# Kernel optimization log

Hardware: AMD Instinct MI355X
Metric: run time of the kernel (lower is better)

The kernel has to match this reference:

```python
import jax, jax.numpy as jnp
import numpy as np

PAD = 8192          # padding index == bloom_filter_dim
H1, H2 = 512, 64
B, K, L = 32, 32, 128


def prelu(x, alpha):
    return jnp.where(x >= 0, x, alpha * x)


def embedding_bag_mean(w, idx):
    # EmbeddingBag(mode='mean', padding_idx=PAD): mean over non-padding entries
    emb = w[idx]                                   # [..., L, H1]
    m = (idx != PAD)[..., None].astype(w.dtype)    # [..., L, 1]
    s = (emb * m).sum(axis=-2)
    cnt = m.sum(axis=-2)
    return jnp.where(cnt > 0, s / jnp.maximum(cnt, 1.0), 0.0)


def hidden_layers(x, W1, b1, W2, b2, a0, a1, a2):
    # PReLU -> Linear -> PReLU -> Linear -> PReLU
    h = prelu(x, a0)
    h = prelu(h @ W1 + b1, a1)
    h = prelu(h @ W2 + b2, a2)
    return h


def setup_inputs() -> dict:
    key = jax.random.key(0)
    ks = jax.random.split(key, 16)
    f = lambda i, shape: jax.random.normal(ks[i], shape, dtype=jnp.float32) * 0.05
    s = lambda v: jnp.asarray(v, dtype=jnp.float32)
    return {
        'query_bloom_filter': jax.random.randint(ks[0], (B, L), 0, PAD),
        'poi_bloom_filter': jax.random.randint(ks[1], (B, K, L), 0, PAD),
        'query_loc': jax.random.normal(ks[2], (B, 2), dtype=jnp.float32),
        'poi_loc': jax.random.normal(ks[3], (B, K, 2), dtype=jnp.float32),
        'codebook_w': f(4, (PAD + 1, H1)),
        'q_W1': f(5, (H1, H2)), 'q_b1': f(6, (H2,)),
        'q_W2': f(7, (H2, H2)), 'q_b2': f(8, (H2,)),
        'p_W1': f(9, (H1, H2)), 'p_b1': f(10, (H2,)),
        'p_W2': f(11, (H2, H2)), 'p_b2': f(12, (H2,)),
        'q_eval_w': f(13, (PAD + 1, H2)),
        'p_eval_w': f(14, (PAD + 1, H2)),
        'q_a0': s(0.25), 'q_a1': s(0.25), 'q_a2': s(0.25),
        'p_a0': s(0.25), 'p_a1': s(0.25), 'p_a2': s(0.25),
        'ind_a': s(0.25),
        'a': s(1.0), 'b': s(0.0), 'c': s(1.0), 'd': s(0.0),
    }


def reference(query_bloom_filter, poi_bloom_filter, query_loc, poi_loc,
              codebook_w, q_W1, q_b1, q_W2, q_b2, p_W1, p_b1, p_W2, p_b2,
              q_eval_w, p_eval_w, q_a0, q_a1, q_a2, p_a0, p_a1, p_a2,
              ind_a, a, b, c, d):
    # --- dense towers ---
    query_embedding = embedding_bag_mean(codebook_w, query_bloom_filter)      # [B, H1]
    query_hidden = hidden_layers(query_embedding, q_W1, q_b1, q_W2, q_b2,
                                 q_a0, q_a1, q_a2)                            # [B, H2]
    poi_embedding = embedding_bag_mean(codebook_w, poi_bloom_filter)          # [B, K, H1]
    poi_hidden = hidden_layers(poi_embedding, p_W1, p_b1, p_W2, p_b2,
                               p_a0, p_a1, p_a2)                              # [B, K, H2]

    # --- bloom-filter intersection (isin_cuda): q element present in poi set ---
    q = query_bloom_filter[:, None, :]                                        # [B, 1, L]
    p = poi_bloom_filter                                                      # [B, K, L]
    match = (q[..., :, None] == p[..., None, :]) & (p[..., None, :] != PAD)   # [B, K, L, L]
    intersection_mask = match.any(axis=-1)                                    # [B, K, L]
    intersection = jnp.where(intersection_mask, q, PAD)                       # [B, K, L]

    # --- sparse term weights via evaluator gathers + mul-sum ---
    q_cols = q_eval_w[intersection]                                           # [B, K, L, H2]
    p_cols = p_eval_w[intersection]                                           # [B, K, L, H2]
    q_sw = prelu(jnp.einsum('bh,bklh->bkl', query_hidden, q_cols), ind_a) + 1.0
    p_sw = prelu(jnp.einsum('bkh,bklh->bkl', poi_hidden, p_cols), ind_a) + 1.0

    text_sim = jnp.where(intersection_mask, q_sw * p_sw, 0.0).sum(axis=-1)    # [B, K]

    # --- location similarity ---
    dist = jnp.sqrt(((query_loc[:, None, :] - poi_loc) ** 2).sum(axis=-1))    # [B, K]
    dist_sim = -jnp.log(dist + 1.0)

    # --- text-sim normalization + relevance ---
    max_sim = text_sim.max(axis=-1, keepdims=True)
    text_sim = (2.0 * text_sim - max_sim) / (max_sim + 1e-6)
    relevance_score = (c - jax.nn.sigmoid(a * text_sim + b)) * (dist_sim - d)
    return relevance_score
```

## Files before the change

### kernel.cpp

```cpp
#include <hip/hip_runtime.h>

#define PAD_V 8192
#define H1 512
#define H2 64
#define B_SZ 32
#define K_SZ 32
#define L_SZ 128
#define EMB_BLOCKS (B_SZ + B_SZ * K_SZ)
#define ISECT_BLOCKS ((B_SZ * K_SZ) / 4)

__global__ __launch_bounds__(512, 4) void front_kernel(
    const int* __restrict__ qbf, const int* __restrict__ pbf,
    const float* __restrict__ codebook,
    const float* __restrict__ qW1, const float* __restrict__ qb1,
    const float* __restrict__ qW2, const float* __restrict__ qb2,
    const float* __restrict__ pW1, const float* __restrict__ pb1,
    const float* __restrict__ pW2, const float* __restrict__ pb2,
    const float* __restrict__ qa0p, const float* __restrict__ qa1p, const float* __restrict__ qa2p,
    const float* __restrict__ pa0p, const float* __restrict__ pa1p, const float* __restrict__ pa2p,
    float* __restrict__ qh_out, float* __restrict__ ph_out,
    int* __restrict__ nh_ws, int* __restrict__ hits_ws)
{
    const int tid = threadIdx.x;

    if (blockIdx.x >= EMB_BLOCKS) {
        __shared__ unsigned int bm4[4][256];
        __shared__ int s_nh4[4];
        __shared__ int s_hit4[4][L_SZ];

        const int pair0 = (blockIdx.x - EMB_BLOCKS) * 4;
        const int sub = tid >> 7;
        const int t   = tid & 127;
        const int pair = pair0 + sub;
        const int b = pair >> 5;

        bm4[sub][t] = 0u; bm4[sub][t + 128] = 0u;
        if (t == 0) s_nh4[sub] = 0;
        __syncthreads();

        int pv = pbf[pair * L_SZ + t];
        if ((unsigned)pv < (unsigned)PAD_V)
            atomicOr(&bm4[sub][pv >> 5], 1u << (pv & 31));
        __syncthreads();

        int v = qbf[b * L_SZ + t];
        bool hit = ((unsigned)v < (unsigned)PAD_V) &&
                   ((bm4[sub][v >> 5] >> (v & 31)) & 1u);
        if (hit) {
            int pos = atomicAdd(&s_nh4[sub], 1);
            s_hit4[sub][pos] = v;
        }
        __syncthreads();

        if (t == 0) nh_ws[pair] = s_nh4[sub];
        if (t < s_nh4[sub]) hits_ws[pair * L_SZ + t] = s_hit4[sub][t];
        return;
    }

    const bool is_q = (blockIdx.x < B_SZ);
    const int* idx_base;
    int bag;
    const float *W1, *b1, *W2, *b2;
    float a0, a1, a2;
    float* out;
    if (is_q) {
        idx_base = qbf; bag = blockIdx.x;
        W1 = qW1; b1 = qb1; W2 = qW2; b2 = qb2;
        a0 = *qa0p; a1 = *qa1p; a2 = *qa2p;
        out = qh_out;
    } else {
        idx_base = pbf; bag = blockIdx.x - B_SZ;
        W1 = pW1; b1 = pb1; W2 = pW2; b2 = pb2;
        a0 = *pa0p; a1 = *pa1p; a2 = *pa2p;
        out = ph_out;
    }

    __shared__ int   s_idx[L_SZ];
    __shared__ int   s_cntp[2];
    __shared__ float s_red[3][L_SZ][4];
    __shared__ float s_x[H1];
    __shared__ float s_p1[32][H2];
    __shared__ float s_h1[H2];

    if (tid < L_SZ) s_idx[tid] = idx_base[bag * L_SZ + tid];
    __syncthreads();

    if (tid < L_SZ) {
        unsigned long long bal = __ballot(s_idx[tid] != PAD_V);
        if ((tid & 63) == 0) s_cntp[tid >> 6] = __popcll(bal);
    }

    const int g = tid & 127;
    const int q = tid >> 7;
    const float4* cb4 = (const float4*)codebook;
    float ax = 0.f, ay = 0.f, az = 0.f, aw = 0.f;
    {
        int   idx[8];
        float4 buf[8];
        #pragma unroll
        for (int batch = 0; batch < 4; batch++) {
            #pragma unroll
            for (int j = 0; j < 8; j++) idx[j] = s_idx[q * 32 + batch * 8 + j];
            #pragma unroll
            for (int j = 0; j < 8; j++) buf[j] = cb4[(size_t)idx[j] * 128 + g];
            #pragma unroll
            for (int j = 0; j < 8; j++) {
                float m = (idx[j] != PAD_V) ? 1.0f : 0.0f;
                ax = fmaf(m, buf[j].x, ax);
                ay = fmaf(m, buf[j].y, ay);
                az = fmaf(m, buf[j].z, az);
                aw = fmaf(m, buf[j].w, aw);
            }
        }
    }
    if (q != 0) {
        s_red[q - 1][g][0] = ax; s_red[q - 1][g][1] = ay;
        s_red[q - 1][g][2] = az; s_red[q - 1][g][3] = aw;
    }
    __syncthreads();
    if (q == 0) {
        int cnt = s_cntp[0] + s_cntp[1];
        float inv = (cnt > 0) ? 1.0f / (float)cnt : 0.0f;
        float e0 = (ax + s_red[0][g][0] + s_red[1][g][0] + s_red[2][g][0]) * inv;
        float e1 = (ay + s_red[0][g][1] + s_red[1][g][1] + s_red[2][g][1]) * inv;
        float e2 = (az + s_red[0][g][2] + s_red[1][g][2] + s_red[2][g][2]) * inv;
        float e3 = (aw + s_red[0][g][3] + s_red[1][g][3] + s_red[2][g][3]) * inv;
        s_x[4 * g + 0] = (e0 >= 0.f) ? e0 : a0 * e0;
        s_x[4 * g + 1] = (e1 >= 0.f) ? e1 : a0 * e1;
        s_x[4 * g + 2] = (e2 >= 0.f) ? e2 : a0 * e2;
        s_x[4 * g + 3] = (e3 >= 0.f) ? e3 : a0 * e3;
    }
    __syncthreads();

    const int j4 = tid & 15;
    const int ch = tid >> 4;
    const float4* W1v = (const float4*)W1;
    {
        const int i0 = ch * 16;
        float sx = 0.f, sy = 0.f, sz = 0.f, sw = 0.f;
        #pragma unroll
        for (int i = 0; i < 16; i++) {
            float x = s_x[i0 + i];
            float4 w = W1v[(size_t)(i0 + i) * 16 + j4];
            sx = fmaf(x, w.x, sx);
            sy = fmaf(x, w.y, sy);
            sz = fmaf(x, w.z, sz);
            sw = fmaf(x, w.w, sw);
        }
        s_p1[ch][4 * j4 + 0] = sx;
        s_p1[ch][4 * j4 + 1] = sy;
        s_p1[ch][4 * j4 + 2] = sz;
        s_p1[ch][4 * j4 + 3] = sw;
    }
    __syncthreads();
    if (tid < H2) {
        float s = b1[tid];
        #pragma unroll
        for (int r = 0; r < 32; r++) s += s_p1[r][tid];
        s_h1[tid] = (s >= 0.f) ? s : a1 * s;
    }
    __syncthreads();

    const float4* W2v = (const float4*)W2;
    {
        const int i0 = ch * 2;
        float sx = 0.f, sy = 0.f, sz = 0.f, sw = 0.f;
        #pragma unroll
        for (int i = 0; i < 2; i++) {
            float x = s_h1[i0 + i];
            float4 w = W2v[(size_t)(i0 + i) * 16 + j4];
            sx = fmaf(x, w.x, sx);
            sy = fmaf(x, w.y, sy);
            sz = fmaf(x, w.z, sz);
            sw = fmaf(x, w.w, sw);
        }
        s_p1[ch][4 * j4 + 0] = sx;
        s_p1[ch][4 * j4 + 1] = sy;
        s_p1[ch][4 * j4 + 2] = sz;
        s_p1[ch][4 * j4 + 3] = sw;
    }
    __syncthreads();
    if (tid < H2) {
        float s = b2[tid];
        #pragma unroll
        for (int r = 0; r < 32; r++) s += s_p1[r][tid];
        s = (s >= 0.f) ? s : a2 * s;
        out[bag * H2 + tid] = s;
    }
}

__global__ __launch_bounds__(64) void text_sim_kernel(
    const float* __restrict__ q_eval, const float* __restrict__ p_eval,
    const float* __restrict__ qh_ws, const float* __restrict__ ph_ws,
    const int* __restrict__ nh_ws, const int* __restrict__ hits_ws,
    const float* __restrict__ ind_ap,
    float* __restrict__ text_out)
{
    const int blk = blockIdx.x;
    const int b    = blk >> 5;
    const int lane = threadIdx.x;

    const float qh = qh_ws[b * H2 + lane];
    const float ph = ph_ws[blk * H2 + lane];
    const int   nh = nh_ws[blk];
    const float ind_a = *ind_ap;

    float local = 0.f;
    for (int hh = 0; hh < nh; hh++) {
        int v = hits_ws[blk * L_SZ + hh];
        float qd = qh * q_eval[(size_t)v * H2 + lane];
        float pd = ph * p_eval[(size_t)v * H2 + lane];
        #pragma unroll
        for (int m = 1; m < 64; m <<= 1) {
            qd += __shfl_xor(qd, m);
            pd += __shfl_xor(pd, m);
        }
        qd = (qd >= 0.f) ? qd : ind_a * qd;
        pd = (pd >= 0.f) ? pd : ind_a * pd;
        local += (qd + 1.f) * (pd + 1.f);
    }
    if (lane == 0) text_out[blk] = local;
}

__global__ __launch_bounds__(64) void epilogue_kernel(
    const float* __restrict__ text_ws,
    const float* __restrict__ qloc, const float* __restrict__ ploc,
    const float* __restrict__ ap, const float* __restrict__ bp,
    const float* __restrict__ cp, const float* __restrict__ dp,
    float* __restrict__ out)
{
    const int b = blockIdx.x;
    const int t = threadIdx.x;
    const int kk = t & 31;

    float ts_raw = text_ws[b * K_SZ + kk];
    float mx = ts_raw;
    #pragma unroll
    for (int m = 1; m < 32; m <<= 1) mx = fmaxf(mx, __shfl_xor(mx, m));

    float qx = qloc[b * 2], qy = qloc[b * 2 + 1];
    float px = ploc[(b * K_SZ + kk) * 2];
    float py = ploc[(b * K_SZ + kk) * 2 + 1];
    float dx = qx - px, dy = qy - py;
    float dist = sqrtf(dx * dx + dy * dy);
    float ds = -logf(dist + 1.0f);

    float ts = (2.0f * ts_raw - mx) / (mx + 1e-6f);
    float A = *ap, Bb = *bp, C = *cp, D = *dp;
    float sig = 1.0f / (1.0f + expf(-(A * ts + Bb)));
    if (t < 32) out[b * K_SZ + kk] = (C - sig) * (ds - D);
}

extern "C" void kernel_launch(void* const* d_in, const int* in_sizes, int n_in,
                              void* d_out, int out_size, void* d_ws, size_t ws_size,
                              hipStream_t stream) {
    const int*   qbf      = (const int*)d_in[0];
    const int*   pbf      = (const int*)d_in[1];
    const float* qloc     = (const float*)d_in[2];
    const float* ploc     = (const float*)d_in[3];
    const float* codebook = (const float*)d_in[4];
    const float* qW1      = (const float*)d_in[5];
    const float* qb1      = (const float*)d_in[6];
    const float* qW2      = (const float*)d_in[7];
    const float* qb2      = (const float*)d_in[8];
    const float* pW1      = (const float*)d_in[9];
    const float* pb1      = (const float*)d_in[10];
    const float* pW2      = (const float*)d_in[11];
    const float* pb2      = (const float*)d_in[12];
    const float* q_eval   = (const float*)d_in[13];
    const float* p_eval   = (const float*)d_in[14];
    const float* qa0      = (const float*)d_in[15];
    const float* qa1      = (const float*)d_in[16];
    const float* qa2      = (const float*)d_in[17];
    const float* pa0      = (const float*)d_in[18];
    const float* pa1      = (const float*)d_in[19];
    const float* pa2      = (const float*)d_in[20];
    const float* ind_a    = (const float*)d_in[21];
    const float* a        = (const float*)d_in[22];
    const float* bsc      = (const float*)d_in[23];
    const float* c        = (const float*)d_in[24];
    const float* d        = (const float*)d_in[25];

    float* qh   = (float*)d_ws;
    float* ph   = qh + B_SZ * H2;
    float* text = ph + B_SZ * K_SZ * H2;
    int*   nh   = (int*)(text + B_SZ * K_SZ);
    int*   hits = nh + B_SZ * K_SZ;

    front_kernel<<<EMB_BLOCKS + ISECT_BLOCKS, 512, 0, stream>>>(
        qbf, pbf, codebook,
        qW1, qb1, qW2, qb2, pW1, pb1, pW2, pb2,
        qa0, qa1, qa2, pa0, pa1, pa2,
        qh, ph, nh, hits);

    text_sim_kernel<<<B_SZ * K_SZ, 64, 0, stream>>>(
        q_eval, p_eval, qh, ph, nh, hits, ind_a, text);

    epilogue_kernel<<<B_SZ, 64, 0, stream>>>(
        text, qloc, ploc, a, bsc, c, d, (float*)d_out);
}
```

Before: 157.3 us.

## Split fused front kernel into sliced gather kernel and separate MLP kernel

Splits the embedding-bag gather from the MLP tower. The gather now runs as 8 column-slice blocks per bag with 256 threads each, which gives far more blocks and more memory-level parallelism across the codebook reads. The mean-pooled PReLU activations go to a workspace buffer, and a separate MLP kernel with 256 threads per block reads them back. The intersection blocks now handle 2 pairs each instead of 4. The cost is an extra kernel launch and a global round-trip for the 512-wide activations.

```diff
diff --git a/kernel.cpp b/kernel.cpp
--- a/kernel.cpp
+++ b/kernel.cpp
@@ -6,140 +6,164 @@
 #define B_SZ 32
 #define K_SZ 32
 #define L_SZ 128
-#define EMB_BLOCKS (B_SZ + B_SZ * K_SZ)
-#define ISECT_BLOCKS ((B_SZ * K_SZ) / 4)
-
-__global__ __launch_bounds__(512, 4) void front_kernel(
+#define NBAGS (B_SZ + B_SZ * K_SZ)
+#define NSLICE 8
+#define GATHER_BLOCKS (NBAGS * NSLICE)
+#define ISECT2_BLOCKS ((B_SZ * K_SZ) / 2)
+
+
+__global__ __launch_bounds__(256, 4) void gather_kernel(
     const int* __restrict__ qbf, const int* __restrict__ pbf,
     const float* __restrict__ codebook,
+    const float* __restrict__ qa0p, const float* __restrict__ pa0p,
+    float* __restrict__ x_ws,
+    int* __restrict__ nh_ws, int* __restrict__ hits_ws)
+{
+    const int tid = threadIdx.x;
+
+    if (blockIdx.x >= GATHER_BLOCKS) {
+        __shared__ unsigned int bm2[2][256];
+        __shared__ int s_nh2[2];
+        __shared__ int s_hit2[2][L_SZ];
+
+        const int pair0 = (blockIdx.x - GATHER_BLOCKS) * 2;
+        const int sub = tid >> 7;
+        const int t   = tid & 127;
+        const int pair = pair0 + sub;
+        const int b = pair >> 5;
+
+        bm2[sub][t] = 0u; bm2[sub][t + 128] = 0u;
+        if (t == 0) s_nh2[sub] = 0;
+        __syncthreads();
+
+        int pv = pbf[pair * L_SZ + t];
+        if ((unsigned)pv < (unsigned)PAD_V)
+            atomicOr(&bm2[sub][pv >> 5], 1u << (pv & 31));
+        __syncthreads();
+
+        int v = qbf[b * L_SZ + t];
+        bool hit = ((unsigned)v < (unsigned)PAD_V) &&
+                   ((bm2[sub][v >> 5] >> (v & 31)) & 1u);
+        if (hit) {
+            int pos = atomicAdd(&s_nh2[sub], 1);
+            s_hit2[sub][pos] = v;
+        }
+        __syncthreads();
+
+        if (t == 0) nh_ws[pair] = s_nh2[sub];
+        if (t < s_nh2[sub]) hits_ws[pair * L_SZ + t] = s_hit2[sub][t];
+        return;
+    }
+
+    const int slice = blockIdx.x & (NSLICE - 1);
+    const int bag   = blockIdx.x >> 3;
+    const bool is_q = (bag < B_SZ);
+    const int* idx_base = is_q ? qbf : pbf;
+    const int  bagl     = is_q ? bag : (bag - B_SZ);
+    const float a0      = is_q ? *qa0p : *pa0p;
+
+    __shared__ int   s_idx[L_SZ];
+    __shared__ int   s_cnt[2];
+    __shared__ float4 s_part[16][16];
+
+    if (tid < L_SZ) {
+        int v = idx_base[bagl * L_SZ + tid];
+        s_idx[tid] = v;
+        unsigned long long bal = __ballot(v != PAD_V);
+        if ((tid & 63) == 0) s_cnt[tid >> 6] = __popcll(bal);
+    }
+    __syncthreads();
+
+    const int c  = tid & 15;
+    const int r0 = tid >> 4;
+    const int gc = slice * 16 + c;
+    const float4* cb4 = (const float4*)codebook;
+
+    float ax = 0.f, ay = 0.f, az = 0.f, aw = 0.f;
+    {
+        int    idx[8];
+        float4 buf[8];
+        #pragma unroll
+        for (int j = 0; j < 8; j++) idx[j] = s_idx[r0 * 8 + j];
+        #pragma unroll
+        for (int j = 0; j < 8; j++) buf[j] = cb4[(size_t)idx[j] * 128 + gc];
+        #pragma unroll
+        for (int j = 0; j < 8; j++) {
+            float m = (idx[j] != PAD_V) ? 1.0f : 0.0f;
+            ax = fmaf(m, buf[j].x, ax);
+            ay = fmaf(m, buf[j].y, ay);
+            az = fmaf(m, buf[j].z, az);
+            aw = fmaf(m, buf[j].w, aw);
+        }
+    }
+    s_part[r0][c] = make_float4(ax, ay, az, aw);
+    __syncthreads();
+
+    if (tid < 16) {
+        int cnt = s_cnt[0] + s_cnt[1];
+        float inv = (cnt > 0) ? 1.0f / (float)cnt : 0.0f;
+        float e0 = 0.f, e1 = 0.f, e2 = 0.f, e3 = 0.f;
+        #pragma unroll
+        for (int r = 0; r < 16; r++) {
+            float4 p = s_part[r][tid];
+            e0 += p.x; e1 += p.y; e2 += p.z; e3 += p.w;
+        }
+        e0 *= inv; e1 *= inv; e2 *= inv; e3 *= inv;
+        float4 o;
+        o.x = (e0 >= 0.f) ? e0 : a0 * e0;
+        o.y = (e1 >= 0.f) ? e1 : a0 * e1;
+        o.z = (e2 >= 0.f) ? e2 : a0 * e2;
+        o.w = (e3 >= 0.f) ? e3 : a0 * e3;
+        ((float4*)x_ws)[(size_t)bag * 128 + slice * 16 + tid] = o;
+    }
+}
+
+__global__ __launch_bounds__(256, 8) void mlp_kernel(
+    const float* __restrict__ x_ws,
     const float* __restrict__ qW1, const float* __restrict__ qb1,
     const float* __restrict__ qW2, const float* __restrict__ qb2,
     const float* __restrict__ pW1, const float* __restrict__ pb1,
     const float* __restrict__ pW2, const float* __restrict__ pb2,
-    const float* __restrict__ qa0p, const float* __restrict__ qa1p, const float* __restrict__ qa2p,
-    const float* __restrict__ pa0p, const float* __restrict__ pa1p, const float* __restrict__ pa2p,
-    float* __restrict__ qh_out, float* __restrict__ ph_out,
-    int* __restrict__ nh_ws, int* __restrict__ hits_ws)
+    const float* __restrict__ qa1p, const float* __restrict__ qa2p,
+    const float* __restrict__ pa1p, const float* __restrict__ pa2p,
+    float* __restrict__ qh_out, float* __restrict__ ph_out)
 {
     const int tid = threadIdx.x;
-
-    if (blockIdx.x >= EMB_BLOCKS) {
-        __shared__ unsigned int bm4[4][256];
-        __shared__ int s_nh4[4];
-        __shared__ int s_hit4[4][L_SZ];
-
-        const int pair0 = (blockIdx.x - EMB_BLOCKS) * 4;
-        const int sub = tid >> 7;
-        const int t   = tid & 127;
-        const int pair = pair0 + sub;
-        const int b = pair >> 5;
-
-        bm4[sub][t] = 0u; bm4[sub][t + 128] = 0u;
-        if (t == 0) s_nh4[sub] = 0;
-        __syncthreads();
-
-        int pv = pbf[pair * L_SZ + t];
-        if ((unsigned)pv < (unsigned)PAD_V)
-            atomicOr(&bm4[sub][pv >> 5], 1u << (pv & 31));
-        __syncthreads();
-
-        int v = qbf[b * L_SZ + t];
-        bool hit = ((unsigned)v < (unsigned)PAD_V) &&
-                   ((bm4[sub][v >> 5] >> (v & 31)) & 1u);
-        if (hit) {
-            int pos = atomicAdd(&s_nh4[sub], 1);
-            s_hit4[sub][pos] = v;
-        }
-        __syncthreads();
-
-        if (t == 0) nh_ws[pair] = s_nh4[sub];
-        if (t < s_nh4[sub]) hits_ws[pair * L_SZ + t] = s_hit4[sub][t];
-        return;
-    }
-
-    const bool is_q = (blockIdx.x < B_SZ);
-    const int* idx_base;
-    int bag;
+    const int bag = blockIdx.x;
+    const bool is_q = (bag < B_SZ);
     const float *W1, *b1, *W2, *b2;
-    float a0, a1, a2;
+    float a1, a2;
     float* out;
+    int bagl;
     if (is_q) {
-        idx_base = qbf; bag = blockIdx.x;
+        bagl = bag;
         W1 = qW1; b1 = qb1; W2 = qW2; b2 = qb2;
-        a0 = *qa0p; a1 = *qa1p; a2 = *qa2p;
+        a1 = *qa1p; a2 = *qa2p;
         out = qh_out;
     } else {
-        idx_base = pbf; bag = blockIdx.x - B_SZ;
+        bagl = bag - B_SZ;
         W1 = pW1; b1 = pb1; W2 = pW2; b2 = pb2;
-        a0 = *pa0p; a1 = *pa1p; a2 = *pa2p;
+        a1 = *pa1p; a2 = *pa2p;
         out = ph_out;
     }
 
-    __shared__ int   s_idx[L_SZ];
-    __shared__ int   s_cntp[2];
-    __shared__ float s_red[3][L_SZ][4];
     __shared__ float s_x[H1];
-    __shared__ float s_p1[32][H2];
+    __shared__ float s_p1[16][H2];
     __shared__ float s_h1[H2];
 
-    if (tid < L_SZ) s_idx[tid] = idx_base[bag * L_SZ + tid];
-    __syncthreads();
-
-    if (tid < L_SZ) {
-        unsigned long long bal = __ballot(s_idx[tid] != PAD_V);
-        if ((tid & 63) == 0) s_cntp[tid >> 6] = __popcll(bal);
-    }
-
-    const int g = tid & 127;
-    const int q = tid >> 7;
-    const float4* cb4 = (const float4*)codebook;
-    float ax = 0.f, ay = 0.f, az = 0.f, aw = 0.f;
-    {
-        int   idx[8];
-        float4 buf[8];
-        #pragma unroll
-        for (int batch = 0; batch < 4; batch++) {
-            #pragma unroll
-            for (int j = 0; j < 8; j++) idx[j] = s_idx[q * 32 + batch * 8 + j];
-            #pragma unroll
-            for (int j = 0; j < 8; j++) buf[j] = cb4[(size_t)idx[j] * 128 + g];
-            #pragma unroll
-            for (int j = 0; j < 8; j++) {
-                float m = (idx[j] != PAD_V) ? 1.0f : 0.0f;
-                ax = fmaf(m, buf[j].x, ax);
-                ay = fmaf(m, buf[j].y, ay);
-                az = fmaf(m, buf[j].z, az);
-                aw = fmaf(m, buf[j].w, aw);
-            }
-        }
-    }
-    if (q != 0) {
-        s_red[q - 1][g][0] = ax; s_red[q - 1][g][1] = ay;
-        s_red[q - 1][g][2] = az; s_red[q - 1][g][3] = aw;
-    }
-    __syncthreads();
-    if (q == 0) {
-        int cnt = s_cntp[0] + s_cntp[1];
-        float inv = (cnt > 0) ? 1.0f / (float)cnt : 0.0f;
-        float e0 = (ax + s_red[0][g][0] + s_red[1][g][0] + s_red[2][g][0]) * inv;
-        float e1 = (ay + s_red[0][g][1] + s_red[1][g][1] + s_red[2][g][1]) * inv;
-        float e2 = (az + s_red[0][g][2] + s_red[1][g][2] + s_red[2][g][2]) * inv;
-        float e3 = (aw + s_red[0][g][3] + s_red[1][g][3] + s_red[2][g][3]) * inv;
-        s_x[4 * g + 0] = (e0 >= 0.f) ? e0 : a0 * e0;
-        s_x[4 * g + 1] = (e1 >= 0.f) ? e1 : a0 * e1;
-        s_x[4 * g + 2] = (e2 >= 0.f) ? e2 : a0 * e2;
-        s_x[4 * g + 3] = (e3 >= 0.f) ? e3 : a0 * e3;
-    }
+    if (tid < 128)
+        ((float4*)s_x)[tid] = ((const float4*)x_ws)[(size_t)bag * 128 + tid];
     __syncthreads();
 
     const int j4 = tid & 15;
     const int ch = tid >> 4;
-    const float4* W1v = (const float4*)W1;
+
     {
-        const int i0 = ch * 16;
+        const float4* W1v = (const float4*)W1;
+        const int i0 = ch * 32;
         float sx = 0.f, sy = 0.f, sz = 0.f, sw = 0.f;
-        #pragma unroll
-        for (int i = 0; i < 16; i++) {
+        #pragma unroll 8
+        for (int i = 0; i < 32; i++) {
             float x = s_x[i0 + i];
             float4 w = W1v[(size_t)(i0 + i) * 16 + j4];
             sx = fmaf(x, w.x, sx);
@@ -156,17 +180,17 @@
     if (tid < H2) {
         float s = b1[tid];
         #pragma unroll
-        for (int r = 0; r < 32; r++) s += s_p1[r][tid];
+        for (int r = 0; r < 16; r++) s += s_p1[r][tid];
         s_h1[tid] = (s >= 0.f) ? s : a1 * s;
     }
     __syncthreads();
 
-    const float4* W2v = (const float4*)W2;
     {
-        const int i0 = ch * 2;
+        const float4* W2v = (const float4*)W2;
+        const int i0 = ch * 4;
         float sx = 0.f, sy = 0.f, sz = 0.f, sw = 0.f;
         #pragma unroll
-        for (int i = 0; i < 2; i++) {
+        for (int i = 0; i < 4; i++) {
             float x = s_h1[i0 + i];
             float4 w = W2v[(size_t)(i0 + i) * 16 + j4];
             sx = fmaf(x, w.x, sx);
@@ -183,9 +207,9 @@
     if (tid < H2) {
         float s = b2[tid];
         #pragma unroll
-        for (int r = 0; r < 32; r++) s += s_p1[r][tid];
+        for (int r = 0; r < 16; r++) s += s_p1[r][tid];
         s = (s >= 0.f) ? s : a2 * s;
-        out[bag * H2 + tid] = s;
+        out[bagl * H2 + tid] = s;
     }
 }
 
@@ -286,12 +310,14 @@
     float* text = ph + B_SZ * K_SZ * H2;
     int*   nh   = (int*)(text + B_SZ * K_SZ);
     int*   hits = nh + B_SZ * K_SZ;
-
-    front_kernel<<<EMB_BLOCKS + ISECT_BLOCKS, 512, 0, stream>>>(
-        qbf, pbf, codebook,
-        qW1, qb1, qW2, qb2, pW1, pb1, pW2, pb2,
-        qa0, qa1, qa2, pa0, pa1, pa2,
-        qh, ph, nh, hits);
+    float* x_ws = (float*)(hits + B_SZ * K_SZ * L_SZ);
+
+    gather_kernel<<<GATHER_BLOCKS + ISECT2_BLOCKS, 256, 0, stream>>>(
+        qbf, pbf, codebook, qa0, pa0, x_ws, nh, hits);
+
+    mlp_kernel<<<NBAGS, 256, 0, stream>>>(
+        x_ws, qW1, qb1, qW2, qb2, pW1, pb1, pW2, pb2,
+        qa1, qa2, pa1, pa2, qh, ph);
 
     text_sim_kernel<<<B_SZ * K_SZ, 64, 0, stream>>>(
         q_eval, p_eval, qh, ph, nh, hits, ind_a, text);
```

New measurement: 145.2 us. 7.7% less time.
